# Kernel optimization log

Hardware: AMD Instinct MI355X
Metric: run time of the kernel (lower is better)

The kernel has to match this reference:

```python
import jax, jax.numpy as jnp
import numpy as np

IN_DIM = 128
OUT_DIM = 128


def setup_inputs() -> dict:
    key = jax.random.key(0)
    k1, k2, k3, k4, k5, k6 = jax.random.split(key, 6)
    B, N, F, K = 4, 20000, IN_DIM, 16
    x = jax.random.normal(k1, (B, N, F), dtype=jnp.float32)
    adj = jax.random.randint(k2, (B, N, K), 0, N, dtype=jnp.int64)
    lim = 1.0 / np.sqrt(IN_DIM)
    W_self = jax.random.uniform(k3, (IN_DIM, OUT_DIM), jnp.float32, -lim, lim)
    b_self = jax.random.uniform(k4, (OUT_DIM,), jnp.float32, -lim, lim)
    W_nei = jax.random.uniform(k5, (IN_DIM, OUT_DIM), jnp.float32, -lim, lim)
    b_nei = jax.random.uniform(k6, (OUT_DIM,), jnp.float32, -lim, lim)
    return {"x": x, "adj": adj, "W_self": W_self, "b_self": b_self,
            "W_nei": W_nei, "b_nei": b_nei}


def reference(x, adj, W_self, b_self, W_nei, b_nei):
    # x: [B,N,F], adj: [B,N,K] indices into N
    # gather neighbor features per batch: [B,N,K,F]
    nei = jax.vmap(lambda xb, ab: xb[ab])(x, adj)
    nei_feat = nei.mean(axis=2)  # [B,N,F]
    out = jnp.einsum('bnf,fo->bno', x, W_self) + b_self \
        + jnp.einsum('bnf,fo->bno', nei_feat, W_nei) + b_nei
    return jax.nn.relu(out)
```

## Files before the change

kernel.cpp:

```cpp
#include <hip/hip_runtime.h>
#include <hip/hip_bf16.h>

#define NBATCH 4
#define NNODE  20000
#define NF     128
#define NK     16
#define BM     64
#define NROWS  (NBATCH * NNODE)
#define NBLK   (NROWS / BM)
#define WTF_BYTES 65536
#define XB16_OFF  WTF_BYTES

typedef __attribute__((ext_vector_type(8))) short bf16x8_t;
typedef __attribute__((ext_vector_type(4))) float f32x4_t;

__device__ __forceinline__ unsigned short f2bf(float f) {
  unsigned int u = __float_as_uint(f);
  u += 0x7fffu + ((u >> 16) & 1u);
  return (unsigned short)(u >> 16);
}

__device__ __forceinline__ int swz(int row, int kbyte) {
  return (row << 9) + (kbyte ^ ((row & 31) << 4));
}

__global__ __launch_bounds__(256) void sage_prep_kernel(
    const float* __restrict__ x, const float* __restrict__ Wself,
    const float* __restrict__ Wnei, unsigned char* __restrict__ ws)
{
  const int bid = blockIdx.x;
  const int tid = threadIdx.x;
  if (bid < 2048) {
    const float4* xv = reinterpret_cast<const float4*>(x);
    uint2* xb = reinterpret_cast<uint2*>(ws + XB16_OFF);
    const int total = NROWS * NF / 4;
    for (int c = bid * 256 + tid; c < total; c += 2048 * 256) {
      const float4 v = xv[c];
      uint2 p;
      p.x = (unsigned int)f2bf(v.x) | ((unsigned int)f2bf(v.y) << 16);
      p.y = (unsigned int)f2bf(v.z) | ((unsigned int)f2bf(v.w) << 16);
      xb[c] = p;
    }
  } else {
    const int ft = (bid - 2048) * 256 + tid;
    const int c = ft >> 9;
    const int s = (ft >> 6) & 7;
    const int l = ft & 63;
    const int col = c * 16 + (l & 15);
    const int k0 = s * 32 + ((l >> 4) << 3);
    unsigned int w[4];
#pragma unroll
    for (int jj = 0; jj < 4; ++jj) {
      const int ka = k0 + jj * 2, kb = k0 + jj * 2 + 1;
      const float va = (ka < NF) ? Wself[ka * NF + col] : Wnei[(ka - NF) * NF + col];
      const float vb = (kb < NF) ? Wself[kb * NF + col] : Wnei[(kb - NF) * NF + col];
      w[jj] = (unsigned int)f2bf(va) | ((unsigned int)f2bf(vb) << 16);
    }
    *reinterpret_cast<uint4*>(ws + (size_t)ft * 16) = make_uint4(w[0], w[1], w[2], w[3]);
  }
}

__global__ __launch_bounds__(256) void sage_fused_kernel(
    const unsigned char* __restrict__ ws, const int* __restrict__ adj,
    const float* __restrict__ bself, const float* __restrict__ bnei,
    float* __restrict__ out)
{
  __shared__ __align__(16) unsigned char sA[BM * 512];

  const int tid  = threadIdx.x;
  const int lane = tid & 63;
  const int wid  = tid >> 6;

  const int orig = blockIdx.x;
  const int xcd = orig & 7, i = orig >> 3;
  const int q = NBLK / 8, r = NBLK % 8;
  const int bid = (xcd < r ? xcd * (q + 1) : r * (q + 1) + (xcd - r) * q) + i;
  const int row0 = bid * BM;

  const unsigned char* xb16 = ws + XB16_OFF;

  {
    const int kb = (tid & 15) * 16;
#pragma unroll
    for (int it = 0; it < 4; ++it) {
      const int rr = it * 16 + (tid >> 4);
      const uint4 v = *reinterpret_cast<const uint4*>(
          xb16 + (size_t)(row0 + rr) * 256 + kb);
      *reinterpret_cast<uint4*>(sA + swz(rr, kb)) = v;
    }
  }

  {
    const int fg = (lane & 15) * 16;
#pragma unroll
    for (int it = 0; it < 4; ++it) {
      const int rr = wid * 16 + it * 4 + (lane >> 4);
      const int gr = row0 + rr;
      const int b  = gr / NNODE;
      const unsigned char* xbb = xb16 + (size_t)b * NNODE * 256;
      const int4* a4 = reinterpret_cast<const int4*>(adj + (size_t)gr * NK);
      float a0=0,a1=0,a2=0,a3=0,a4f=0,a5=0,a6=0,a7=0;
#pragma unroll
      for (int kk = 0; kk < 4; ++kk) {
        const int4 idx = a4[kk];
        const int id[4] = {idx.x, idx.y, idx.z, idx.w};
#pragma unroll
        for (int m = 0; m < 4; ++m) {
          const uint4 v = *reinterpret_cast<const uint4*>(
              xbb + (size_t)id[m] * 256 + fg);
          a0 += __uint_as_float(v.x << 16);
          a1 += __uint_as_float(v.x & 0xffff0000u);
          a2 += __uint_as_float(v.y << 16);
          a3 += __uint_as_float(v.y & 0xffff0000u);
          a4f += __uint_as_float(v.z << 16);
          a5 += __uint_as_float(v.z & 0xffff0000u);
          a6 += __uint_as_float(v.w << 16);
          a7 += __uint_as_float(v.w & 0xffff0000u);
        }
      }
      const float sc = 1.f / 16.f;
      uint4 p;
      p.x = (unsigned int)f2bf(a0*sc) | ((unsigned int)f2bf(a1*sc) << 16);
      p.y = (unsigned int)f2bf(a2*sc) | ((unsigned int)f2bf(a3*sc) << 16);
      p.z = (unsigned int)f2bf(a4f*sc) | ((unsigned int)f2bf(a5*sc) << 16);
      p.w = (unsigned int)f2bf(a6*sc) | ((unsigned int)f2bf(a7*sc) << 16);
      *reinterpret_cast<uint4*>(sA + swz(rr, 256 + fg)) = p;
    }
  }

  __syncthreads();

  const int frow = lane & 15;
  const int kgrp = lane >> 4;

  f32x4_t acc[8];
#pragma unroll
  for (int c = 0; c < 8; ++c) acc[c] = (f32x4_t){0.f, 0.f, 0.f, 0.f};

  bf16x8_t afr[8];
#pragma unroll
  for (int s = 0; s < 8; ++s) {
    const int kb = s * 64 + kgrp * 16;
    afr[s] = *reinterpret_cast<const bf16x8_t*>(sA + swz(wid * 16 + frow, kb));
  }

  const bf16x8_t* wtf = reinterpret_cast<const bf16x8_t*>(ws);
#pragma unroll
  for (int c = 0; c < 8; ++c) {
#pragma unroll
    for (int s = 0; s < 8; ++s) {
      const bf16x8_t bfr = wtf[(c * 8 + s) * 64 + lane];
      acc[c] = __builtin_amdgcn_mfma_f32_16x16x32_bf16(afr[s], bfr, acc[c], 0, 0, 0);
    }
  }

#pragma unroll
  for (int c = 0; c < 8; ++c) {
    const int col  = c * 16 + frow;
    const float bias = bself[col] + bnei[col];
#pragma unroll
    for (int j = 0; j < 4; ++j) {
      const int rr = wid * 16 + kgrp * 4 + j;
      const float v = acc[c][j] + bias;
      out[(size_t)(row0 + rr) * NF + col] = fmaxf(v, 0.f);
    }
  }
}

extern "C" void kernel_launch(void* const* d_in, const int* in_sizes, int n_in,
                              void* d_out, int out_size, void* d_ws, size_t ws_size,
                              hipStream_t stream) {
  const float* x     = (const float*)d_in[0];
  const int*   adj   = (const int*)d_in[1];
  const float* Wself = (const float*)d_in[2];
  const float* bself = (const float*)d_in[3];
  const float* Wnei  = (const float*)d_in[4];
  const float* bnei  = (const float*)d_in[5];
  float* out = (float*)d_out;
  unsigned char* ws = (unsigned char*)d_ws;

  hipLaunchKernelGGL(sage_prep_kernel, dim3(2064), dim3(256), 0, stream,
                     x, Wself, Wnei, ws);
  hipLaunchKernelGGL(sage_fused_kernel, dim3(NBLK), dim3(256), 0, stream,
                     ws, adj, bself, bnei, out);
}
```

Measured before the change: 49.09 us.

## Halve row tile, batch neighbor gathers, split MFMA columns across waves

Shrinks the per-block row tile from 64 to 32 rows, which doubles the block count, and sets an occupancy hint of 8 blocks per CU. The neighbor gather now has 8 lanes per row, each covering two half-feature chunks, and issues all 16 neighbor loads before accumulating, to expose more memory-level parallelism. The MFMA stage splits 2 row tiles x 2 column halves across the 4 waves, and outputs use nontemporal stores. The costs are more register pressure from the 16 outstanding uint4 loads and twice as many blocks reloading the weight fragments.

```diff
diff --git a/kernel.cpp b/kernel.cpp
--- a/kernel.cpp
+++ b/kernel.cpp
@@ -5,7 +5,7 @@
 #define NNODE  20000
 #define NF     128
 #define NK     16
-#define BM     64
+#define BM     32
 #define NROWS  (NBATCH * NNODE)
 #define NBLK   (NROWS / BM)
 #define WTF_BYTES 65536
@@ -60,7 +60,7 @@
   }
 }
 
-__global__ __launch_bounds__(256) void sage_fused_kernel(
+__global__ __launch_bounds__(256, 8) void sage_fused_kernel(
     const unsigned char* __restrict__ ws, const int* __restrict__ adj,
     const float* __restrict__ bself, const float* __restrict__ bnei,
     float* __restrict__ out)
@@ -82,7 +82,7 @@
   {
     const int kb = (tid & 15) * 16;
 #pragma unroll
-    for (int it = 0; it < 4; ++it) {
+    for (int it = 0; it < 2; ++it) {
       const int rr = it * 16 + (tid >> 4);
       const uint4 v = *reinterpret_cast<const uint4*>(
           xb16 + (size_t)(row0 + rr) * 256 + kb);
@@ -91,40 +91,48 @@
   }
 
   {
-    const int fg = (lane & 15) * 16;
+    const int fh   = (lane & 7) * 16;
+    const int rsub = lane >> 3;
+    const int rr   = wid * 8 + rsub;
+    const int gr   = row0 + rr;
+    const int b    = gr / NNODE;
+    const unsigned char* xbb = xb16 + (size_t)b * NNODE * 256;
+    const int4* a4 = reinterpret_cast<const int4*>(adj + (size_t)gr * NK);
+
+    int idx[16];
 #pragma unroll
-    for (int it = 0; it < 4; ++it) {
-      const int rr = wid * 16 + it * 4 + (lane >> 4);
-      const int gr = row0 + rr;
-      const int b  = gr / NNODE;
-      const unsigned char* xbb = xb16 + (size_t)b * NNODE * 256;
-      const int4* a4 = reinterpret_cast<const int4*>(adj + (size_t)gr * NK);
+    for (int kk = 0; kk < 4; ++kk) {
+      const int4 t = a4[kk];
+      idx[kk * 4 + 0] = t.x; idx[kk * 4 + 1] = t.y;
+      idx[kk * 4 + 2] = t.z; idx[kk * 4 + 3] = t.w;
+    }
+
+#pragma unroll
+    for (int h = 0; h < 2; ++h) {
+      const int off = h * 128 + fh;
+      uint4 v[16];
+#pragma unroll
+      for (int k = 0; k < 16; ++k)
+        v[k] = *reinterpret_cast<const uint4*>(xbb + (size_t)idx[k] * 256 + off);
       float a0=0,a1=0,a2=0,a3=0,a4f=0,a5=0,a6=0,a7=0;
 #pragma unroll
-      for (int kk = 0; kk < 4; ++kk) {
-        const int4 idx = a4[kk];
-        const int id[4] = {idx.x, idx.y, idx.z, idx.w};
-#pragma unroll
-        for (int m = 0; m < 4; ++m) {
-          const uint4 v = *reinterpret_cast<const uint4*>(
-              xbb + (size_t)id[m] * 256 + fg);
-          a0 += __uint_as_float(v.x << 16);
-          a1 += __uint_as_float(v.x & 0xffff0000u);
-          a2 += __uint_as_float(v.y << 16);
-          a3 += __uint_as_float(v.y & 0xffff0000u);
-          a4f += __uint_as_float(v.z << 16);
-          a5 += __uint_as_float(v.z & 0xffff0000u);
-          a6 += __uint_as_float(v.w << 16);
-          a7 += __uint_as_float(v.w & 0xffff0000u);
-        }
+      for (int k = 0; k < 16; ++k) {
+        a0  += __uint_as_float(v[k].x << 16);
+        a1  += __uint_as_float(v[k].x & 0xffff0000u);
+        a2  += __uint_as_float(v[k].y << 16);
+        a3  += __uint_as_float(v[k].y & 0xffff0000u);
+        a4f += __uint_as_float(v[k].z << 16);
+        a5  += __uint_as_float(v[k].z & 0xffff0000u);
+        a6  += __uint_as_float(v[k].w << 16);
+        a7  += __uint_as_float(v[k].w & 0xffff0000u);
       }
       const float sc = 1.f / 16.f;
       uint4 p;
-      p.x = (unsigned int)f2bf(a0*sc) | ((unsigned int)f2bf(a1*sc) << 16);
-      p.y = (unsigned int)f2bf(a2*sc) | ((unsigned int)f2bf(a3*sc) << 16);
+      p.x = (unsigned int)f2bf(a0*sc)  | ((unsigned int)f2bf(a1*sc) << 16);
+      p.y = (unsigned int)f2bf(a2*sc)  | ((unsigned int)f2bf(a3*sc) << 16);
       p.z = (unsigned int)f2bf(a4f*sc) | ((unsigned int)f2bf(a5*sc) << 16);
-      p.w = (unsigned int)f2bf(a6*sc) | ((unsigned int)f2bf(a7*sc) << 16);
-      *reinterpret_cast<uint4*>(sA + swz(rr, 256 + fg)) = p;
+      p.w = (unsigned int)f2bf(a6*sc)  | ((unsigned int)f2bf(a7*sc) << 16);
+      *reinterpret_cast<uint4*>(sA + swz(rr, 256 + off)) = p;
     }
   }
 
@@ -132,37 +140,41 @@
 
   const int frow = lane & 15;
   const int kgrp = lane >> 4;
+  const int mrow = (wid & 1) * 16;
+  const int cb   = wid >> 1;
 
-  f32x4_t acc[8];
+  f32x4_t acc[4];
 #pragma unroll
-  for (int c = 0; c < 8; ++c) acc[c] = (f32x4_t){0.f, 0.f, 0.f, 0.f};
+  for (int c = 0; c < 4; ++c) acc[c] = (f32x4_t){0.f, 0.f, 0.f, 0.f};
 
   bf16x8_t afr[8];
 #pragma unroll
   for (int s = 0; s < 8; ++s) {
     const int kb = s * 64 + kgrp * 16;
-    afr[s] = *reinterpret_cast<const bf16x8_t*>(sA + swz(wid * 16 + frow, kb));
+    afr[s] = *reinterpret_cast<const bf16x8_t*>(sA + swz(mrow + frow, kb));
   }
 
   const bf16x8_t* wtf = reinterpret_cast<const bf16x8_t*>(ws);
 #pragma unroll
-  for (int c = 0; c < 8; ++c) {
+  for (int c = 0; c < 4; ++c) {
+    const int gc = cb * 4 + c;
 #pragma unroll
     for (int s = 0; s < 8; ++s) {
-      const bf16x8_t bfr = wtf[(c * 8 + s) * 64 + lane];
+      const bf16x8_t bfr = wtf[(gc * 8 + s) * 64 + lane];
       acc[c] = __builtin_amdgcn_mfma_f32_16x16x32_bf16(afr[s], bfr, acc[c], 0, 0, 0);
     }
   }
 
 #pragma unroll
-  for (int c = 0; c < 8; ++c) {
-    const int col  = c * 16 + frow;
+  for (int c = 0; c < 4; ++c) {
+    const int gc  = cb * 4 + c;
+    const int col = gc * 16 + frow;
     const float bias = bself[col] + bnei[col];
 #pragma unroll
     for (int j = 0; j < 4; ++j) {
-      const int rr = wid * 16 + kgrp * 4 + j;
-      const float v = acc[c][j] + bias;
-      out[(size_t)(row0 + rr) * NF + col] = fmaxf(v, 0.f);
+      const int rr = mrow + kgrp * 4 + j;
+      const float v = fmaxf(acc[c][j] + bias, 0.f);
+      __builtin_nontemporal_store(v, &out[(size_t)(row0 + rr) * NF + col]);
     }
   }
 }
```

After: 86.12 us. +75.4%, slower.

## Gather neighbor features from an FP8 copy of x to halve gather traffic

Applied to the files above, without the earlier changes.

The prep kernel now also writes an FP8-quantized copy of x, and the neighbor-mean gather reads 128-byte FP8 rows instead of 256-byte bf16 rows, unpacking with hardware fp8-to-f32 conversions. Each lane now covers 16 features, and eight neighbor loads are issued together to raise memory-level parallelism. The aim is to cut random-gather bandwidth, which dominates the fused kernel. In exchange, prep writes an extra 10 MB, and FP8 quantization of neighbor features adds noticeable numerical error that may exceed the tolerance.

```diff
diff --git a/kernel.cpp b/kernel.cpp
--- a/kernel.cpp
+++ b/kernel.cpp
@@ -10,14 +10,16 @@
 #define NBLK   (NROWS / BM)
 #define WTF_BYTES 65536
 #define XB16_OFF  WTF_BYTES
+#define XF8_OFF   (XB16_OFF + NROWS * NF * 2)
 
 typedef __attribute__((ext_vector_type(8))) short bf16x8_t;
 typedef __attribute__((ext_vector_type(4))) float f32x4_t;
-
-__device__ __forceinline__ unsigned short f2bf(float f) {
+typedef __attribute__((ext_vector_type(2))) float f32x2_t;
+
+__device__ __forceinline__ unsigned int f2bf(float f) {
   unsigned int u = __float_as_uint(f);
   u += 0x7fffu + ((u >> 16) & 1u);
-  return (unsigned short)(u >> 16);
+  return u >> 16;
 }
 
 __device__ __forceinline__ int swz(int row, int kbyte) {
@@ -33,13 +35,18 @@
   if (bid < 2048) {
     const float4* xv = reinterpret_cast<const float4*>(x);
     uint2* xb = reinterpret_cast<uint2*>(ws + XB16_OFF);
+    unsigned int* x8 = reinterpret_cast<unsigned int*>(ws + XF8_OFF);
     const int total = NROWS * NF / 4;
     for (int c = bid * 256 + tid; c < total; c += 2048 * 256) {
       const float4 v = xv[c];
       uint2 p;
-      p.x = (unsigned int)f2bf(v.x) | ((unsigned int)f2bf(v.y) << 16);
-      p.y = (unsigned int)f2bf(v.z) | ((unsigned int)f2bf(v.w) << 16);
+      p.x = f2bf(v.x) | (f2bf(v.y) << 16);
+      p.y = f2bf(v.z) | (f2bf(v.w) << 16);
       xb[c] = p;
+      int p8 = 0;
+      p8 = __builtin_amdgcn_cvt_pk_fp8_f32(v.x, v.y, p8, false);
+      p8 = __builtin_amdgcn_cvt_pk_fp8_f32(v.z, v.w, p8, true);
+      x8[c] = (unsigned int)p8;
     }
   } else {
     const int ft = (bid - 2048) * 256 + tid;
@@ -54,7 +61,7 @@
       const int ka = k0 + jj * 2, kb = k0 + jj * 2 + 1;
       const float va = (ka < NF) ? Wself[ka * NF + col] : Wnei[(ka - NF) * NF + col];
       const float vb = (kb < NF) ? Wself[kb * NF + col] : Wnei[(kb - NF) * NF + col];
-      w[jj] = (unsigned int)f2bf(va) | ((unsigned int)f2bf(vb) << 16);
+      w[jj] = f2bf(va) | (f2bf(vb) << 16);
     }
     *reinterpret_cast<uint4*>(ws + (size_t)ft * 16) = make_uint4(w[0], w[1], w[2], w[3]);
   }
@@ -78,6 +85,7 @@
   const int row0 = bid * BM;
 
   const unsigned char* xb16 = ws + XB16_OFF;
+  const unsigned char* xf8  = ws + XF8_OFF;
 
   {
     const int kb = (tid & 15) * 16;
@@ -91,40 +99,62 @@
   }
 
   {
-    const int fg = (lane & 15) * 16;
-#pragma unroll
-    for (int it = 0; it < 4; ++it) {
-      const int rr = wid * 16 + it * 4 + (lane >> 4);
+    const int fg   = (lane & 7) * 16;
+    const int rsub = lane >> 3;
+#pragma unroll
+    for (int pass = 0; pass < 2; ++pass) {
+      const int rr = wid * 16 + pass * 8 + rsub;
       const int gr = row0 + rr;
       const int b  = gr / NNODE;
-      const unsigned char* xbb = xb16 + (size_t)b * NNODE * 256;
+      const unsigned char* xbb = xf8 + (size_t)b * NNODE * 128 + fg;
       const int4* a4 = reinterpret_cast<const int4*>(adj + (size_t)gr * NK);
-      float a0=0,a1=0,a2=0,a3=0,a4f=0,a5=0,a6=0,a7=0;
-#pragma unroll
-      for (int kk = 0; kk < 4; ++kk) {
-        const int4 idx = a4[kk];
-        const int id[4] = {idx.x, idx.y, idx.z, idx.w};
-#pragma unroll
-        for (int m = 0; m < 4; ++m) {
-          const uint4 v = *reinterpret_cast<const uint4*>(
-              xbb + (size_t)id[m] * 256 + fg);
-          a0 += __uint_as_float(v.x << 16);
-          a1 += __uint_as_float(v.x & 0xffff0000u);
-          a2 += __uint_as_float(v.y << 16);
-          a3 += __uint_as_float(v.y & 0xffff0000u);
-          a4f += __uint_as_float(v.z << 16);
-          a5 += __uint_as_float(v.z & 0xffff0000u);
-          a6 += __uint_as_float(v.w << 16);
-          a7 += __uint_as_float(v.w & 0xffff0000u);
+
+      float acc16[16];
+#pragma unroll
+      for (int k = 0; k < 16; ++k) acc16[k] = 0.f;
+
+#pragma unroll
+      for (int half = 0; half < 2; ++half) {
+        const int4 t0 = a4[half * 2 + 0];
+        const int4 t1 = a4[half * 2 + 1];
+        uint4 v[8];
+        v[0] = *reinterpret_cast<const uint4*>(xbb + (size_t)t0.x * 128);
+        v[1] = *reinterpret_cast<const uint4*>(xbb + (size_t)t0.y * 128);
+        v[2] = *reinterpret_cast<const uint4*>(xbb + (size_t)t0.z * 128);
+        v[3] = *reinterpret_cast<const uint4*>(xbb + (size_t)t0.w * 128);
+        v[4] = *reinterpret_cast<const uint4*>(xbb + (size_t)t1.x * 128);
+        v[5] = *reinterpret_cast<const uint4*>(xbb + (size_t)t1.y * 128);
+        v[6] = *reinterpret_cast<const uint4*>(xbb + (size_t)t1.z * 128);
+        v[7] = *reinterpret_cast<const uint4*>(xbb + (size_t)t1.w * 128);
+#define UNPK(word, base)                                                  \
+        {                                                                 \
+          f32x2_t lo = __builtin_amdgcn_cvt_pk_f32_fp8((word), false);    \
+          f32x2_t hi = __builtin_amdgcn_cvt_pk_f32_fp8((word), true);     \
+          acc16[(base) + 0] += lo[0]; acc16[(base) + 1] += lo[1];         \
+          acc16[(base) + 2] += hi[0]; acc16[(base) + 3] += hi[1];         \
         }
+#pragma unroll
+        for (int k = 0; k < 8; ++k) {
+          UNPK(v[k].x, 0)
+          UNPK(v[k].y, 4)
+          UNPK(v[k].z, 8)
+          UNPK(v[k].w, 12)
+        }
+#undef UNPK
       }
       const float sc = 1.f / 16.f;
-      uint4 p;
-      p.x = (unsigned int)f2bf(a0*sc) | ((unsigned int)f2bf(a1*sc) << 16);
-      p.y = (unsigned int)f2bf(a2*sc) | ((unsigned int)f2bf(a3*sc) << 16);
-      p.z = (unsigned int)f2bf(a4f*sc) | ((unsigned int)f2bf(a5*sc) << 16);
-      p.w = (unsigned int)f2bf(a6*sc) | ((unsigned int)f2bf(a7*sc) << 16);
-      *reinterpret_cast<uint4*>(sA + swz(rr, 256 + fg)) = p;
+      uint4 p0, p1;
+      p0.x = f2bf(acc16[0]*sc)  | (f2bf(acc16[1]*sc)  << 16);
+      p0.y = f2bf(acc16[2]*sc)  | (f2bf(acc16[3]*sc)  << 16);
+      p0.z = f2bf(acc16[4]*sc)  | (f2bf(acc16[5]*sc)  << 16);
+      p0.w = f2bf(acc16[6]*sc)  | (f2bf(acc16[7]*sc)  << 16);
+      p1.x = f2bf(acc16[8]*sc)  | (f2bf(acc16[9]*sc)  << 16);
+      p1.y = f2bf(acc16[10]*sc) | (f2bf(acc16[11]*sc) << 16);
+      p1.z = f2bf(acc16[12]*sc) | (f2bf(acc16[13]*sc) << 16);
+      p1.w = f2bf(acc16[14]*sc) | (f2bf(acc16[15]*sc) << 16);
+      const int kb = 256 + fg * 2;
+      *reinterpret_cast<uint4*>(sA + swz(rr, kb))      = p0;
+      *reinterpret_cast<uint4*>(sA + swz(rr, kb + 16)) = p1;
     }
   }
 
```

New measurement: 46.33 us. -5.6%, faster.

## Project before gathering: GEMM x into self and FP8 neighbor projections, then gather

Applied to the files above, without the earlier changes.

The work is reordered using linearity of the mean: x is first multiplied by both weight matrices in one GEMM. The self projection plus bias is stored as bf16 and the neighbor projection as FP8. A separate kernel then gathers 16 FP8 neighbor rows per node, averages them, adds the self term and applies ReLU. This removes the separate x-to-bf16 conversion pass and halves the bytes fetched per random gather, but it adds an extra kernel and intermediate buffers and loses accuracy from FP8 storage of projected values.

```diff
diff --git a/kernel.cpp b/kernel.cpp
--- a/kernel.cpp
+++ b/kernel.cpp
@@ -5,165 +5,185 @@
 #define NNODE  20000
 #define NF     128
 #define NK     16
-#define BM     64
 #define NROWS  (NBATCH * NNODE)
-#define NBLK   (NROWS / BM)
+#define NBLK   1250
 #define WTF_BYTES 65536
-#define XB16_OFF  WTF_BYTES
+#define BIAS_OFF  WTF_BYTES
+#define S_OFF     (WTF_BYTES + 1024)
+#define Y_OFF     (S_OFF + NROWS * NF * 2)
 
 typedef __attribute__((ext_vector_type(8))) short bf16x8_t;
 typedef __attribute__((ext_vector_type(4))) float f32x4_t;
-
-__device__ __forceinline__ unsigned short f2bf(float f) {
+typedef __attribute__((ext_vector_type(2))) float f32x2_t;
+
+__device__ __forceinline__ unsigned int f2bf(float f) {
   unsigned int u = __float_as_uint(f);
   u += 0x7fffu + ((u >> 16) & 1u);
-  return (unsigned short)(u >> 16);
-}
-
-__device__ __forceinline__ int swz(int row, int kbyte) {
-  return (row << 9) + (kbyte ^ ((row & 31) << 4));
-}
-
-__global__ __launch_bounds__(256) void sage_prep_kernel(
-    const float* __restrict__ x, const float* __restrict__ Wself,
-    const float* __restrict__ Wnei, unsigned char* __restrict__ ws)
+  return u >> 16;
+}
+
+__device__ __forceinline__ int xcd_swz(int orig) {
+  const int xcd = orig & 7, i = orig >> 3;
+  const int q = NBLK / 8, r = NBLK % 8;
+  return (xcd < r ? xcd * (q + 1) : r * (q + 1) + (xcd - r) * q) + i;
+}
+
+__global__ __launch_bounds__(256) void sage_wprep(
+    const float* __restrict__ Ws, const float* __restrict__ bs,
+    const float* __restrict__ Wn, const float* __restrict__ bn,
+    unsigned char* __restrict__ ws)
 {
-  const int bid = blockIdx.x;
-  const int tid = threadIdx.x;
-  if (bid < 2048) {
-    const float4* xv = reinterpret_cast<const float4*>(x);
-    uint2* xb = reinterpret_cast<uint2*>(ws + XB16_OFF);
-    const int total = NROWS * NF / 4;
-    for (int c = bid * 256 + tid; c < total; c += 2048 * 256) {
-      const float4 v = xv[c];
-      uint2 p;
-      p.x = (unsigned int)f2bf(v.x) | ((unsigned int)f2bf(v.y) << 16);
-      p.y = (unsigned int)f2bf(v.z) | ((unsigned int)f2bf(v.w) << 16);
-      xb[c] = p;
-    }
-  } else {
-    const int ft = (bid - 2048) * 256 + tid;
-    const int c = ft >> 9;
-    const int s = (ft >> 6) & 7;
-    const int l = ft & 63;
-    const int col = c * 16 + (l & 15);
-    const int k0 = s * 32 + ((l >> 4) << 3);
-    unsigned int w[4];
-#pragma unroll
-    for (int jj = 0; jj < 4; ++jj) {
-      const int ka = k0 + jj * 2, kb = k0 + jj * 2 + 1;
-      const float va = (ka < NF) ? Wself[ka * NF + col] : Wnei[(ka - NF) * NF + col];
-      const float vb = (kb < NF) ? Wself[kb * NF + col] : Wnei[(kb - NF) * NF + col];
-      w[jj] = (unsigned int)f2bf(va) | ((unsigned int)f2bf(vb) << 16);
-    }
-    *reinterpret_cast<uint4*>(ws + (size_t)ft * 16) = make_uint4(w[0], w[1], w[2], w[3]);
-  }
-}
-
-__global__ __launch_bounds__(256) void sage_fused_kernel(
+  const int bid = blockIdx.x, tid = threadIdx.x;
+  if (bid == 16) {
+    if (tid < NF) ((float*)(ws + BIAS_OFF))[tid] = bs[tid] + bn[tid];
+    return;
+  }
+  const int ft = bid * 256 + tid;
+  const int gc = ft >> 8;
+  const int s  = (ft >> 6) & 3;
+  const int l  = ft & 63;
+  const int colg = gc * 16 + (l & 15);
+  const int k0 = s * 32 + ((l >> 4) << 3);
+  const float* W = (colg < NF) ? Ws : Wn;
+  const int col = (colg < NF) ? colg : colg - NF;
+  unsigned int w[4];
+#pragma unroll
+  for (int jj = 0; jj < 4; ++jj) {
+    const float va = W[(k0 + 2 * jj) * NF + col];
+    const float vb = W[(k0 + 2 * jj + 1) * NF + col];
+    w[jj] = f2bf(va) | (f2bf(vb) << 16);
+  }
+  *reinterpret_cast<uint4*>(ws + (size_t)ft * 16) = make_uint4(w[0], w[1], w[2], w[3]);
+}
+
+__global__ __launch_bounds__(256) void sage_gemm(
+    const float* __restrict__ x, unsigned char* __restrict__ ws)
+{
+  const int tid = threadIdx.x, lane = tid & 63, wid = tid >> 6;
+  const int bid = xcd_swz(blockIdx.x);
+  const int row0 = bid * 64 + wid * 16;
+  const int fl = lane & 15, q = lane >> 4;
+
+  bf16x8_t afr[4];
+  const float* xr = x + (size_t)(row0 + fl) * NF + q * 8;
+#pragma unroll
+  for (int s = 0; s < 4; ++s) {
+    const float4 v0 = *reinterpret_cast<const float4*>(xr + s * 32);
+    const float4 v1 = *reinterpret_cast<const float4*>(xr + s * 32 + 4);
+    union { unsigned int u[4]; bf16x8_t v; } r;
+    r.u[0] = f2bf(v0.x) | (f2bf(v0.y) << 16);
+    r.u[1] = f2bf(v0.z) | (f2bf(v0.w) << 16);
+    r.u[2] = f2bf(v1.x) | (f2bf(v1.y) << 16);
+    r.u[3] = f2bf(v1.z) | (f2bf(v1.w) << 16);
+    afr[s] = r.v;
+  }
+
+  f32x4_t acc[16];
+#pragma unroll
+  for (int c = 0; c < 16; ++c) acc[c] = (f32x4_t){0.f, 0.f, 0.f, 0.f};
+
+  const bf16x8_t* wtf = reinterpret_cast<const bf16x8_t*>(ws);
+#pragma unroll
+  for (int c = 0; c < 16; ++c) {
+#pragma unroll
+    for (int s = 0; s < 4; ++s) {
+      acc[c] = __builtin_amdgcn_mfma_f32_16x16x32_bf16(
+          afr[s], wtf[(c * 4 + s) * 64 + lane], acc[c], 0, 0, 0);
+    }
+  }
+
+  const float* bias = reinterpret_cast<const float*>(ws + BIAS_OFF);
+  unsigned short* sp = reinterpret_cast<unsigned short*>(ws + S_OFF);
+  unsigned char*  yp = ws + Y_OFF;
+
+#pragma unroll
+  for (int c = 0; c < 8; ++c) {
+    const int col = c * 16 + fl;
+    const float b = bias[col];
+#pragma unroll
+    for (int j = 0; j < 4; ++j) {
+      const int r = row0 + q * 4 + j;
+      sp[(size_t)r * NF + col] = (unsigned short)f2bf(acc[c][j] + b);
+    }
+  }
+#pragma unroll
+  for (int c = 8; c < 16; ++c) {
+    const int col = (c - 8) * 16 + fl;
+#pragma unroll
+    for (int j = 0; j < 4; ++j) {
+      const int r = row0 + q * 4 + j;
+      const int p8 = __builtin_amdgcn_cvt_pk_fp8_f32(acc[c][j], acc[c][j], 0, false);
+      yp[(size_t)r * NF + col] = (unsigned char)(p8 & 0xff);
+    }
+  }
+}
+
+__global__ __launch_bounds__(256) void sage_finish(
     const unsigned char* __restrict__ ws, const int* __restrict__ adj,
-    const float* __restrict__ bself, const float* __restrict__ bnei,
     float* __restrict__ out)
 {
-  __shared__ __align__(16) unsigned char sA[BM * 512];
-
-  const int tid  = threadIdx.x;
-  const int lane = tid & 63;
-  const int wid  = tid >> 6;
-
-  const int orig = blockIdx.x;
-  const int xcd = orig & 7, i = orig >> 3;
-  const int q = NBLK / 8, r = NBLK % 8;
-  const int bid = (xcd < r ? xcd * (q + 1) : r * (q + 1) + (xcd - r) * q) + i;
-  const int row0 = bid * BM;
-
-  const unsigned char* xb16 = ws + XB16_OFF;
-
-  {
-    const int kb = (tid & 15) * 16;
-#pragma unroll
-    for (int it = 0; it < 4; ++it) {
-      const int rr = it * 16 + (tid >> 4);
-      const uint4 v = *reinterpret_cast<const uint4*>(
-          xb16 + (size_t)(row0 + rr) * 256 + kb);
-      *reinterpret_cast<uint4*>(sA + swz(rr, kb)) = v;
-    }
-  }
-
-  {
-    const int fg = (lane & 15) * 16;
-#pragma unroll
-    for (int it = 0; it < 4; ++it) {
-      const int rr = wid * 16 + it * 4 + (lane >> 4);
-      const int gr = row0 + rr;
-      const int b  = gr / NNODE;
-      const unsigned char* xbb = xb16 + (size_t)b * NNODE * 256;
-      const int4* a4 = reinterpret_cast<const int4*>(adj + (size_t)gr * NK);
-      float a0=0,a1=0,a2=0,a3=0,a4f=0,a5=0,a6=0,a7=0;
-#pragma unroll
-      for (int kk = 0; kk < 4; ++kk) {
-        const int4 idx = a4[kk];
-        const int id[4] = {idx.x, idx.y, idx.z, idx.w};
-#pragma unroll
-        for (int m = 0; m < 4; ++m) {
-          const uint4 v = *reinterpret_cast<const uint4*>(
-              xbb + (size_t)id[m] * 256 + fg);
-          a0 += __uint_as_float(v.x << 16);
-          a1 += __uint_as_float(v.x & 0xffff0000u);
-          a2 += __uint_as_float(v.y << 16);
-          a3 += __uint_as_float(v.y & 0xffff0000u);
-          a4f += __uint_as_float(v.z << 16);
-          a5 += __uint_as_float(v.z & 0xffff0000u);
-          a6 += __uint_as_float(v.w << 16);
-          a7 += __uint_as_float(v.w & 0xffff0000u);
-        }
-      }
-      const float sc = 1.f / 16.f;
-      uint4 p;
-      p.x = (unsigned int)f2bf(a0*sc) | ((unsigned int)f2bf(a1*sc) << 16);
-      p.y = (unsigned int)f2bf(a2*sc) | ((unsigned int)f2bf(a3*sc) << 16);
-      p.z = (unsigned int)f2bf(a4f*sc) | ((unsigned int)f2bf(a5*sc) << 16);
-      p.w = (unsigned int)f2bf(a6*sc) | ((unsigned int)f2bf(a7*sc) << 16);
-      *reinterpret_cast<uint4*>(sA + swz(rr, 256 + fg)) = p;
-    }
-  }
-
-  __syncthreads();
-
-  const int frow = lane & 15;
-  const int kgrp = lane >> 4;
-
-  f32x4_t acc[8];
-#pragma unroll
-  for (int c = 0; c < 8; ++c) acc[c] = (f32x4_t){0.f, 0.f, 0.f, 0.f};
-
-  bf16x8_t afr[8];
-#pragma unroll
-  for (int s = 0; s < 8; ++s) {
-    const int kb = s * 64 + kgrp * 16;
-    afr[s] = *reinterpret_cast<const bf16x8_t*>(sA + swz(wid * 16 + frow, kb));
-  }
-
-  const bf16x8_t* wtf = reinterpret_cast<const bf16x8_t*>(ws);
-#pragma unroll
-  for (int c = 0; c < 8; ++c) {
-#pragma unroll
-    for (int s = 0; s < 8; ++s) {
-      const bf16x8_t bfr = wtf[(c * 8 + s) * 64 + lane];
-      acc[c] = __builtin_amdgcn_mfma_f32_16x16x32_bf16(afr[s], bfr, acc[c], 0, 0, 0);
-    }
-  }
-
-#pragma unroll
-  for (int c = 0; c < 8; ++c) {
-    const int col  = c * 16 + frow;
-    const float bias = bself[col] + bnei[col];
-#pragma unroll
-    for (int j = 0; j < 4; ++j) {
-      const int rr = wid * 16 + kgrp * 4 + j;
-      const float v = acc[c][j] + bias;
-      out[(size_t)(row0 + rr) * NF + col] = fmaxf(v, 0.f);
-    }
+  const int tid = threadIdx.x, lane = tid & 63, wid = tid >> 6;
+  const int bid = xcd_swz(blockIdx.x);
+  const int rg = lane >> 4, fl = lane & 15;
+
+  const unsigned short* sp = reinterpret_cast<const unsigned short*>(ws + S_OFF);
+  const unsigned char*  yp = ws + Y_OFF;
+
+#pragma unroll
+  for (int it = 0; it < 4; ++it) {
+    const int row = bid * 64 + wid * 16 + it * 4 + rg;
+    const int b = row / NNODE;
+    const unsigned char* yb = yp + (size_t)b * NNODE * NF + fl * 8;
+    const int4* a4 = reinterpret_cast<const int4*>(adj + (size_t)row * NK);
+    const int4 t0 = a4[0], t1 = a4[1], t2 = a4[2], t3 = a4[3];
+    const int idx[16] = {t0.x, t0.y, t0.z, t0.w, t1.x, t1.y, t1.z, t1.w,
+                         t2.x, t2.y, t2.z, t2.w, t3.x, t3.y, t3.z, t3.w};
+
+    const uint4 sv = *reinterpret_cast<const uint4*>(sp + (size_t)row * NF + fl * 8);
+
+    float a[8];
+#pragma unroll
+    for (int e = 0; e < 8; ++e) a[e] = 0.f;
+
+#define ACC2(word, base)                                                   \
+    {                                                                      \
+      f32x2_t lo = __builtin_amdgcn_cvt_pk_f32_fp8((word), false);         \
+      f32x2_t hi = __builtin_amdgcn_cvt_pk_f32_fp8((word), true);          \
+      a[(base) + 0] += lo[0]; a[(base) + 1] += lo[1];                      \
+      a[(base) + 2] += hi[0]; a[(base) + 3] += hi[1];                      \
+    }
+#pragma unroll
+    for (int g = 0; g < 4; ++g) {
+      uint2 v0 = *reinterpret_cast<const uint2*>(yb + (size_t)idx[g * 4 + 0] * NF);
+      uint2 v1 = *reinterpret_cast<const uint2*>(yb + (size_t)idx[g * 4 + 1] * NF);
+      uint2 v2 = *reinterpret_cast<const uint2*>(yb + (size_t)idx[g * 4 + 2] * NF);
+      uint2 v3 = *reinterpret_cast<const uint2*>(yb + (size_t)idx[g * 4 + 3] * NF);
+      ACC2(v0.x, 0) ACC2(v0.y, 4)
+      ACC2(v1.x, 0) ACC2(v1.y, 4)
+      ACC2(v2.x, 0) ACC2(v2.y, 4)
+      ACC2(v3.x, 0) ACC2(v3.y, 4)
+    }
+#undef ACC2
+
+    float se[8];
+    se[0] = __uint_as_float(sv.x << 16); se[1] = __uint_as_float(sv.x & 0xffff0000u);
+    se[2] = __uint_as_float(sv.y << 16); se[3] = __uint_as_float(sv.y & 0xffff0000u);
+    se[4] = __uint_as_float(sv.z << 16); se[5] = __uint_as_float(sv.z & 0xffff0000u);
+    se[6] = __uint_as_float(sv.w << 16); se[7] = __uint_as_float(sv.w & 0xffff0000u);
+
+    const float sc = 1.f / 16.f;
+    float4 o0, o1;
+    o0.x = fmaxf(se[0] + a[0] * sc, 0.f);
+    o0.y = fmaxf(se[1] + a[1] * sc, 0.f);
+    o0.z = fmaxf(se[2] + a[2] * sc, 0.f);
+    o0.w = fmaxf(se[3] + a[3] * sc, 0.f);
+    o1.x = fmaxf(se[4] + a[4] * sc, 0.f);
+    o1.y = fmaxf(se[5] + a[5] * sc, 0.f);
+    o1.z = fmaxf(se[6] + a[6] * sc, 0.f);
+    o1.w = fmaxf(se[7] + a[7] * sc, 0.f);
+    float* op = out + (size_t)row * NF + fl * 8;
+    *reinterpret_cast<float4*>(op)     = o0;
+    *reinterpret_cast<float4*>(op + 4) = o1;
   }
 }
 
@@ -179,8 +199,9 @@
   float* out = (float*)d_out;
   unsigned char* ws = (unsigned char*)d_ws;
 
-  hipLaunchKernelGGL(sage_prep_kernel, dim3(2064), dim3(256), 0, stream,
-                     x, Wself, Wnei, ws);
-  hipLaunchKernelGGL(sage_fused_kernel, dim3(NBLK), dim3(256), 0, stream,
-                     ws, adj, bself, bnei, out);
-}
+  hipLaunchKernelGGL(sage_wprep, dim3(17), dim3(256), 0, stream,
+                     Wself, bself, Wnei, bnei, ws);
+  hipLaunchKernelGGL(sage_gemm, dim3(NBLK), dim3(256), 0, stream, x, ws);
+  hipLaunchKernelGGL(sage_finish, dim3(NBLK), dim3(256), 0, stream,
+                     ws, adj, out);
+}
```

Result: slower. 55.42 us (+12.9%).
